# Kernel tuning notes

Hardware: AMD Instinct MI355X
Metric: run time of the kernel (lower is better)

Reference implementation:

```python
import jax, jax.numpy as jnp
import numpy as np

FULL_RANGE = 128
MOOD_DIM = 4
LAYERS = 4
UNITS = 512
MOOD_UNITS = 32


def lstm_layer(x, Wih, Whh, bih, bhh):
    # x: [B, T, I]; torch LSTM gate order: i, f, g, o
    B, T, _ = x.shape
    H = Whh.shape[1]
    xg = jnp.einsum('bti,gi->btg', x, Wih) + bih + bhh  # [B, T, 4H]

    def step(carry, g_t):
        h, c = carry
        g = g_t + h @ Whh.T
        i, f, gc, o = jnp.split(g, 4, axis=-1)
        c = jax.nn.sigmoid(f) * c + jax.nn.sigmoid(i) * jnp.tanh(gc)
        h = jax.nn.sigmoid(o) * jnp.tanh(c)
        return (h, c), h

    h0 = jnp.zeros((B, H), x.dtype)
    (_, _), hs = jax.lax.scan(step, (h0, h0), xg.transpose(1, 0, 2))
    return hs.transpose(1, 0, 2)  # [B, T, H]


def setup_inputs() -> dict:
    key = jax.random.key(0)
    ks = jax.random.split(key, 16)
    s = 0.05
    H4 = 4 * UNITS
    in0 = FULL_RANGE + MOOD_UNITS
    return {
        'inputs': jax.random.normal(ks[0], (16, 1024, FULL_RANGE), jnp.float32),
        'moods': jax.random.normal(ks[1], (16, MOOD_DIM), jnp.float32),
        'W_mood': jax.random.normal(ks[2], (MOOD_UNITS, MOOD_DIM), jnp.float32) * s,
        'b_mood': jnp.zeros((MOOD_UNITS,), jnp.float32),
        'W_ih0': jax.random.normal(ks[3], (H4, in0), jnp.float32) * s,
        'W_hh0': jax.random.normal(ks[4], (H4, UNITS), jnp.float32) * s,
        'b_ih0': jax.random.normal(ks[5], (H4,), jnp.float32) * s,
        'b_hh0': jax.random.normal(ks[6], (H4,), jnp.float32) * s,
        'W_ih_rest': jax.random.normal(ks[7], (LAYERS - 1, H4, UNITS), jnp.float32) * s,
        'W_hh_rest': jax.random.normal(ks[8], (LAYERS - 1, H4, UNITS), jnp.float32) * s,
        'b_ih_rest': jax.random.normal(ks[9], (LAYERS - 1, H4), jnp.float32) * s,
        'b_hh_rest': jax.random.normal(ks[10], (LAYERS - 1, H4), jnp.float32) * s,
        'W_out': jax.random.normal(ks[11], (FULL_RANGE, UNITS), jnp.float32) * s,
        'b_out': jnp.zeros((FULL_RANGE,), jnp.float32),
    }


def reference(inputs, moods, W_mood, b_mood, W_ih0, W_hh0, b_ih0, b_hh0,
              W_ih_rest, W_hh_rest, b_ih_rest, b_hh_rest, W_out, b_out):
    B, S, _ = inputs.shape
    m = moods @ W_mood.T + b_mood                      # [B, MOOD_UNITS]
    m = jnp.broadcast_to(m[:, None, :], (B, S, MOOD_UNITS))
    x = jnp.concatenate([inputs, m], axis=2)           # [B, S, FULL_RANGE+MOOD_UNITS]

    params = [(W_ih0, W_hh0, b_ih0, b_hh0)] + [
        (W_ih_rest[i], W_hh_rest[i], b_ih_rest[i], b_hh_rest[i])
        for i in range(LAYERS - 1)
    ]
    for i, (Wih, Whh, bih, bhh) in enumerate(params):
        prev = x
        d = 2 ** i
        F = x.shape[-1]
        # torch unfold(1,d,d).permute(0,3,1,2).view(B*d, S//d, F):
        # sub-batch (b,k) is the stride-d subsequence with phase k
        xd = x.reshape(B, S // d, d, F).transpose(0, 2, 1, 3).reshape(B * d, S // d, F)
        yd = lstm_layer(xd, Wih, Whh, bih, bhh)         # [B*d, S//d, H]
        x = yd.reshape(B, d, S // d, UNITS).transpose(0, 2, 1, 3).reshape(B, S, UNITS)
        if i > 0:
            x = prev + x
    return x @ W_out.T + b_out                          # [B, S, FULL_RANGE]
```

## Files before the change

kernel.cpp:

```cpp
#include <hip/hip_runtime.h>
#include <stdint.h>

#define DEVFN __device__ __forceinline__
#define SCOPE_AGENT __HIP_MEMORY_SCOPE_AGENT

static constexpr int B_ = 16;
static constexpr int S_ = 1024;
static constexpr int FR = 128;
static constexpr int MU = 32;
static constexpr int H_ = 512;
static constexpr int G4 = 2048;

static constexpr int NCH_WHH = 4 * 64 * 2048;
static constexpr int NCH_WI0 = 16 * 2048;
static constexpr int NCH_WIR = 3 * 64 * 2048;
static constexpr int NCH_TOT = NCH_WHH + NCH_WI0 + NCH_WIR;

static constexpr int HV64 = 128 * 256;

typedef _Float16 h2_t __attribute__((ext_vector_type(2)));

DEVFN uint16_t f2h(float x) { union { _Float16 f; uint16_t u; } c; c.f = (_Float16)x; return c.u; }
DEVFN uint32_t pack_f16(float a, float b) { return (uint32_t)f2h(a) | ((uint32_t)f2h(b) << 16); }

DEVFN float fd2(uint32_t a, uint32_t b, float c) {
#if __has_builtin(__builtin_amdgcn_fdot2)
    return __builtin_amdgcn_fdot2(__builtin_bit_cast(h2_t, a),
                                  __builtin_bit_cast(h2_t, b), c, false);
#else
    asm("v_dot2_f32_f16 %0, %1, %2, %0" : "+v"(c) : "v"(a), "v"(b));
    return c;
#endif
}
DEVFN float dot8f(uint4 w, uint4 x, float s) {
    s = fd2(w.x, x.x, s); s = fd2(w.y, x.y, s);
    s = fd2(w.z, x.z, s); s = fd2(w.w, x.w, s);
    return s;
}
DEVFN float sigm(float x) { return 1.0f / (1.0f + __expf(-x)); }
DEVFN float tanhfast(float x) {
    float e = __expf(2.0f * fabsf(x));
    float r = 1.0f - 2.0f / (e + 1.0f);
    return copysignf(r, x);
}

__global__ __launch_bounds__(256) void mood_kernel(
    const float* __restrict__ moods, const float* __restrict__ W_mood,
    const float* __restrict__ b_mood, const float* __restrict__ W_ih0,
    const float* __restrict__ b_ih0, const float* __restrict__ b_hh0,
    float* __restrict__ mc)
{
    int b = blockIdx.x, tid = threadIdx.x;
    __shared__ float m[MU];
    if (tid < MU) {
        float s = b_mood[tid];
        #pragma unroll
        for (int j = 0; j < 4; j++) s += moods[b * 4 + j] * W_mood[tid * 4 + j];
        m[tid] = s;
    }
    __syncthreads();
    for (int row = tid; row < G4; row += 256) {
        float s = b_ih0[row] + b_hh0[row];
        const float* w = W_ih0 + (size_t)row * (FR + MU) + FR;
        #pragma unroll
        for (int u = 0; u < MU; u++) s += m[u] * w[u];
        mc[(size_t)b * G4 + row] = s;
    }
}

__global__ __launch_bounds__(256) void pack_kernel(
    const float* __restrict__ W_hh0, const float* __restrict__ W_hh_r,
    const float* __restrict__ W_ih0, const float* __restrict__ W_ih_r,
    uint4* __restrict__ pwh, uint4* __restrict__ pwi0, uint4* __restrict__ pwir)
{
    int c = blockIdx.x * 256 + threadIdx.x;
    if (c >= NCH_TOT) return;
    const float* src;
    uint4* dst;
    if (c < NCH_WHH) {
        int l = c >> 17, ck = (c >> 11) & 63, row = c & 2047;
        const float* W = (l == 0) ? W_hh0 : W_hh_r + (size_t)(l - 1) * G4 * H_;
        src = W + (size_t)row * H_ + ck * 8;
        dst = pwh + c;
    } else if (c < NCH_WHH + NCH_WI0) {
        int d = c - NCH_WHH;
        int ck = d >> 11, row = d & 2047;
        src = W_ih0 + (size_t)row * (FR + MU) + ck * 8;
        dst = pwi0 + d;
    } else {
        int e = c - NCH_WHH - NCH_WI0;
        int l = e >> 17, ck = (e >> 11) & 63, row = e & 2047;
        src = W_ih_r + (size_t)l * G4 * H_ + (size_t)row * H_ + ck * 8;
        dst = pwir + e;
    }
    uint4 o;
    o.x = pack_f16(src[0], src[1]);
    o.y = pack_f16(src[2], src[3]);
    o.z = pack_f16(src[4], src[5]);
    o.w = pack_f16(src[6], src[7]);
    *dst = o;
}

#define HSTEP(J) { \
    _Pragma("unroll") \
    for (int b = 0; b < SB; b++) { \
        uint4 hv = *(const uint4*)&lds_h[b][kg * 64 + (J) * 8]; \
        accA[b] = dot8f(h0c##J, hv, accA[b]); \
        accB[b] = dot8f(h1c##J, hv, accB[b]); \
    } }

#define XBODY(J) { \
    uint4 w0 = WI0[(size_t)(J) * G4 + row0]; \
    uint4 w1 = WI0[(size_t)(J) * G4 + row1]; \
    _Pragma("unroll") \
    for (int b = 0; b < SB; b++) { \
        uint4 xv = *(const uint4*)&lds_x[b][kg * (KIN / 8) + (J) * 8]; \
        accA[b] = dot8f(w0, xv, accA[b]); \
        accB[b] = dot8f(w1, xv, accB[b]); \
    } }

template <int LAYER>
__global__ __attribute__((amdgpu_waves_per_eu(2, 2))) __launch_bounds__(512)
void scan_kernel(
    const float* x_in, float* x_out,
    const uint4* __restrict__ pwi, const uint4* __restrict__ pwh,
    const float* __restrict__ biasA, const float* __restrict__ biasB,
    unsigned long long* __restrict__ hb64, uint32_t tagbase)
{
    constexpr int DIL = 1 << LAYER;
    constexpr int SB = DIL;
    constexpr int T = S_ / DIL;
    constexpr int KIN = (LAYER == 0) ? FR : H_;
    constexpr int NJX = KIN / 64;
    constexpr int XTOT = SB * KIN;
    constexpr int XRS = (XTOT + 511) / 512;
    constexpr int KSH = (LAYER == 0) ? 7 : 9;
    constexpr int LOFF = (LAYER == 0) ? 0 : (LAYER - 1);
    constexpr bool WREG = (LAYER <= 1);
    constexpr bool EARLY = (SB <= 4);

    const int bid = blockIdx.x;
    const int g = bid & 15, wgi = bid >> 4;
    const int tid = threadIdx.x;
    const int kg = tid >> 6;
    const int r6 = tid & 63;
    const int gp = r6 >> 5;
    const int um = r6 & 31;
    const int U0 = wgi * 32;
    const int row0 = (2 * gp) * H_ + U0 + um;
    const int row1 = row0 + H_;
    const int rl0 = (2 * gp) * 32 + um, rl1 = rl0 + 32;
    const int sb0 = g * SB;

    __shared__ __align__(16) uint16_t lds_x[SB][KIN];
    __shared__ __align__(16) uint16_t lds_h[SB][H_];
    __shared__ float lds_p[SB][8][132];

    const uint4* WH = pwh + ((size_t)(LAYER * 64 + kg * 8)) * G4;

    uint4 h0c0, h1c0, h0c1, h1c1, h0c2, h1c2, h0c3, h1c3;
    uint4 h0c4, h1c4, h0c5, h1c5, h0c6, h1c6, h0c7, h1c7;
    if constexpr (WREG) {
        h0c0 = WH[(size_t)0 * G4 + row0]; h1c0 = WH[(size_t)0 * G4 + row1];
        h0c1 = WH[(size_t)1 * G4 + row0]; h1c1 = WH[(size_t)1 * G4 + row1];
        h0c2 = WH[(size_t)2 * G4 + row0]; h1c2 = WH[(size_t)2 * G4 + row1];
        h0c3 = WH[(size_t)3 * G4 + row0]; h1c3 = WH[(size_t)3 * G4 + row1];
        h0c4 = WH[(size_t)4 * G4 + row0]; h1c4 = WH[(size_t)4 * G4 + row1];
        h0c5 = WH[(size_t)5 * G4 + row0]; h1c5 = WH[(size_t)5 * G4 + row1];
        h0c6 = WH[(size_t)6 * G4 + row0]; h1c6 = WH[(size_t)6 * G4 + row1];
        h0c7 = WH[(size_t)7 * G4 + row0]; h1c7 = WH[(size_t)7 * G4 + row1];
    }

    const uint4* WI0;
    if constexpr (LAYER == 0) WI0 = pwi + ((size_t)(kg * NJX)) * G4;
    else                      WI0 = pwi + ((size_t)(LOFF * 64 + kg * 8)) * G4;

    const int b0 = tid >> 5, uu = tid & 31;
    const bool upd = tid < SB * 32;
    float biasv[4] = {0.f, 0.f, 0.f, 0.f};
    float cst = 0.0f;
    if (upd) {
        #pragma unroll
        for (int Gx = 0; Gx < 4; Gx++) {
            int RR = Gx * H_ + U0 + uu;
            if constexpr (LAYER == 0)
                biasv[Gx] = biasA[(size_t)(sb0 + b0) * G4 + RR];
            else
                biasv[Gx] = biasA[RR] + biasB[RR];
        }
    }
    const size_t pslot = (size_t)(sb0 + b0) * 256 + ((U0 + uu) >> 1);
    const int usb = sb0 + b0, ubg = usb >> LAYER, uk = usb & (DIL - 1);

    float xsr[XRS];
    #pragma unroll
    for (int rr = 0; rr < XRS; rr++) {
        int idx = tid + rr * 512;
        if (idx < XTOT) {
            int b = idx >> KSH, off = idx & (KIN - 1);
            int sb = sb0 + b, bg = sb >> LAYER, k = sb & (DIL - 1);
            xsr[rr] = x_in[((size_t)bg * S_ + k) * KIN + off];
        }
    }
    asm volatile("s_waitcnt vmcnt(0)" ::: "memory");
    __syncthreads();
    if (upd && ((uu & 1) == 0))
        __hip_atomic_store(hb64 + HV64 + pslot,
                           (unsigned long long)tagbase << 32,
                           __ATOMIC_RELAXED, SCOPE_AGENT);

    for (int t = 0; t < T; t++) {
        #pragma unroll
        for (int rr = 0; rr < XRS; rr++) {
            int idx = tid + rr * 512;
            if (idx < XTOT) lds_x[idx >> KSH][idx & (KIN - 1)] = f2h(xsr[rr]);
        }
        __syncthreads();

        const unsigned long long* hrd = hb64 + (size_t)((t + 1) & 1) * HV64;
        const uint32_t want = tagbase + (uint32_t)t;

        unsigned long long pve[EARLY ? SB : 1];
        if constexpr (EARLY) {
            if (tid < 256) {
                #pragma unroll
                for (int b = 0; b < SB; b++)
                    pve[b] = __hip_atomic_load(hrd + (size_t)(sb0 + b) * 256 + tid,
                                               __ATOMIC_RELAXED, SCOPE_AGENT);
            }
        }

        if (t + 1 < T) {
            #pragma unroll
            for (int rr = 0; rr < XRS; rr++) {
                int idx = tid + rr * 512;
                if (idx < XTOT) {
                    int b = idx >> KSH, off = idx & (KIN - 1);
                    int sb = sb0 + b, bg = sb >> LAYER, k = sb & (DIL - 1);
                    xsr[rr] = x_in[((size_t)bg * S_ + (size_t)(t + 1) * DIL + k) * KIN + off];
                }
            }
        }

        float res = 0.f;
        if constexpr (LAYER > 0) {
            if (upd)
                res = x_in[((size_t)ubg * S_ + (size_t)t * DIL + uk) * H_ + U0 + uu];
        }

        float accA[SB], accB[SB];
        #pragma unroll
        for (int b = 0; b < SB; b++) { accA[b] = 0.f; accB[b] = 0.f; }
        if constexpr (LAYER >= 2) {
            #pragma unroll 4
            for (int j = 0; j < NJX; j++) XBODY(j)
        } else {
            #pragma unroll 2
            for (int j = 0; j < NJX; j++) XBODY(j)
        }

        asm volatile("s_waitcnt vmcnt(0)" ::: "memory");

        if (tid < 256) {
            if constexpr (EARLY) {
                #pragma unroll
                for (int b = 0; b < SB; b++) {
                    unsigned long long v = pve[b];
                    while ((uint32_t)(v >> 32) != want) {
                        __builtin_amdgcn_s_sleep(1);
                        v = __hip_atomic_load(hrd + (size_t)(sb0 + b) * 256 + tid,
                                              __ATOMIC_RELAXED, SCOPE_AGENT);
                    }
                    ((uint32_t*)&lds_h[b][0])[tid] = (uint32_t)v;
                }
            } else {
                unsigned long long pv[SB];
                #pragma unroll
                for (int b = 0; b < SB; b++)
                    pv[b] = __hip_atomic_load(hrd + (size_t)(sb0 + b) * 256 + tid,
                                              __ATOMIC_RELAXED, SCOPE_AGENT);
                #pragma unroll
                for (int b = 0; b < SB; b++) {
                    while ((uint32_t)(pv[b] >> 32) != want) {
                        __builtin_amdgcn_s_sleep(1);
                        pv[b] = __hip_atomic_load(hrd + (size_t)(sb0 + b) * 256 + tid,
                                                  __ATOMIC_RELAXED, SCOPE_AGENT);
                    }
                    ((uint32_t*)&lds_h[b][0])[tid] = (uint32_t)pv[b];
                }
            }
        }
        __syncthreads();

        if constexpr (WREG) {
            HSTEP(0) HSTEP(1) HSTEP(2) HSTEP(3)
            HSTEP(4) HSTEP(5) HSTEP(6) HSTEP(7)
        } else {
            #pragma unroll 4
            for (int j = 0; j < 8; j++) {
                uint4 w0 = WH[(size_t)j * G4 + row0];
                uint4 w1 = WH[(size_t)j * G4 + row1];
                #pragma unroll
                for (int b = 0; b < SB; b++) {
                    uint4 hv = *(const uint4*)&lds_h[b][kg * 64 + j * 8];
                    accA[b] = dot8f(w0, hv, accA[b]);
                    accB[b] = dot8f(w1, hv, accB[b]);
                }
            }
        }

        #pragma unroll
        for (int b = 0; b < SB; b++) {
            lds_p[b][kg][rl0] = accA[b];
            lds_p[b][kg][rl1] = accB[b];
        }
        asm volatile("s_waitcnt vmcnt(0)" ::: "memory");
        __syncthreads();

        if (upd) {
            float gv[4];
            #pragma unroll
            for (int Gx = 0; Gx < 4; Gx++) {
                int rl = Gx * 32 + uu;
                float s = biasv[Gx];
                #pragma unroll
                for (int q = 0; q < 8; q++) s += lds_p[b0][q][rl];
                gv[Gx] = s;
            }
            float ci = sigm(gv[0]), cf = sigm(gv[1]);
            float cg = tanhfast(gv[2]), co = sigm(gv[3]);
            cst = cf * cst + ci * cg;
            float hv = co * tanhfast(cst);
            uint32_t h16 = (uint32_t)f2h(hv);
            uint32_t partner = (uint32_t)__shfl_xor((int)h16, 1);
            if ((uu & 1) == 0)
                __hip_atomic_store(hb64 + (size_t)(t & 1) * HV64 + pslot,
                                   ((unsigned long long)(tagbase + (uint32_t)t + 1) << 32) |
                                   (unsigned long long)(h16 | (partner << 16)),
                                   __ATOMIC_RELAXED, SCOPE_AGENT);
            x_out[((size_t)ubg * S_ + (size_t)t * DIL + uk) * H_ + U0 + uu] = hv + res;
        }
    }
}

__global__ __launch_bounds__(256) void out_gemm(
    const float* __restrict__ x, const float* __restrict__ Wout,
    const float* __restrict__ bout, float* __restrict__ out)
{
    __shared__ __align__(16) float xs[8][H_];
    int tid = threadIdx.x;
    size_t tok0 = (size_t)blockIdx.x * 8;
    const float4* src = (const float4*)(x + tok0 * H_);
    for (int idx = tid; idx < 8 * H_ / 4; idx += 256)
        ((float4*)xs)[idx] = src[idx];
    __syncthreads();

    int col = tid & 127, th = tid >> 7;
    int tb = th * 4;
    float a0 = 0.f, a1 = 0.f, a2 = 0.f, a3 = 0.f;
    const float4* w = (const float4*)(Wout + (size_t)col * H_);
    #pragma unroll 4
    for (int j = 0; j < H_ / 4; j++) {
        float4 wv = w[j];
        float4 x0 = ((const float4*)xs[tb + 0])[j];
        float4 x1 = ((const float4*)xs[tb + 1])[j];
        float4 x2 = ((const float4*)xs[tb + 2])[j];
        float4 x3 = ((const float4*)xs[tb + 3])[j];
        a0 = fmaf(wv.x, x0.x, a0); a0 = fmaf(wv.y, x0.y, a0); a0 = fmaf(wv.z, x0.z, a0); a0 = fmaf(wv.w, x0.w, a0);
        a1 = fmaf(wv.x, x1.x, a1); a1 = fmaf(wv.y, x1.y, a1); a1 = fmaf(wv.z, x1.z, a1); a1 = fmaf(wv.w, x1.w, a1);
        a2 = fmaf(wv.x, x2.x, a2); a2 = fmaf(wv.y, x2.y, a2); a2 = fmaf(wv.z, x2.z, a2); a2 = fmaf(wv.w, x2.w, a2);
        a3 = fmaf(wv.x, x3.x, a3); a3 = fmaf(wv.y, x3.y, a3); a3 = fmaf(wv.z, x3.z, a3); a3 = fmaf(wv.w, x3.w, a3);
    }
    float bo = bout[col];
    out[(tok0 + tb + 0) * FR + col] = a0 + bo;
    out[(tok0 + tb + 1) * FR + col] = a1 + bo;
    out[(tok0 + tb + 2) * FR + col] = a2 + bo;
    out[(tok0 + tb + 3) * FR + col] = a3 + bo;
}

extern "C" void kernel_launch(void* const* d_in, const int* in_sizes, int n_in,
                              void* d_out, int out_size, void* d_ws, size_t ws_size,
                              hipStream_t stream)
{
    const float* inputs = (const float*)d_in[0];
    const float* moods  = (const float*)d_in[1];
    const float* W_mood = (const float*)d_in[2];
    const float* b_mood = (const float*)d_in[3];
    const float* W_ih0  = (const float*)d_in[4];
    const float* W_hh0  = (const float*)d_in[5];
    const float* b_ih0  = (const float*)d_in[6];
    const float* b_hh0  = (const float*)d_in[7];
    const float* W_ih_r = (const float*)d_in[8];
    const float* W_hh_r = (const float*)d_in[9];
    const float* b_ih_r = (const float*)d_in[10];
    const float* b_hh_r = (const float*)d_in[11];
    const float* W_out  = (const float*)d_in[12];
    const float* b_out  = (const float*)d_in[13];

    float* ws = (float*)d_ws;
    float* mc = ws;
    float* xA = ws + 32768;
    unsigned long long* hb64 = (unsigned long long*)(xA + 8388608);
    uint4* pwh  = (uint4*)(hb64 + 2 * HV64);
    uint4* pwi0 = pwh + NCH_WHH;
    uint4* pwir = pwi0 + NCH_WI0;

    (void)hipMemsetAsync(hb64, 0, 2 * HV64 * sizeof(unsigned long long), stream);
    mood_kernel<<<16, 256, 0, stream>>>(moods, W_mood, b_mood, W_ih0, b_ih0, b_hh0, mc);
    pack_kernel<<<(NCH_TOT + 255) / 256, 256, 0, stream>>>(
        W_hh0, W_hh_r, W_ih0, W_ih_r, pwh, pwi0, pwir);

    scan_kernel<0><<<256, 512, 0, stream>>>(inputs, xA, pwi0, pwh, mc, nullptr, hb64, 1u);
    scan_kernel<1><<<256, 512, 0, stream>>>(xA, xA, pwir, pwh,
                                            b_ih_r, b_hh_r, hb64, 1026u);
    scan_kernel<2><<<256, 512, 0, stream>>>(xA, xA, pwir, pwh,
                                            b_ih_r + G4, b_hh_r + G4, hb64, 1539u);
    scan_kernel<3><<<256, 512, 0, stream>>>(xA, xA, pwir, pwh,
                                            b_ih_r + 2 * G4, b_hh_r + 2 * G4, hb64, 1796u);

    out_gemm<<<2048, 256, 0, stream>>>(xA, W_out, b_out, (float*)d_out);
}
```

Before: 5.292 ms.

## Fuse LSTM layer pairs into one launch with flag-based cross-layer pipelining

Merges layers 0+1 and layers 2+3 into single launches of 512 blocks. The first layer of each pair publishes per-timestep progress flags after its atomic output stores, and the second layer spin-waits on those flags before loading its inputs. This lets the dependent layer's recurrence run concurrently with the producer's instead of waiting for a full kernel boundary. The residual input is now staged through LDS, and tags and h-buffers are separated per layer. In exchange, waves-per-EU rises from 2 to 4, which may pressure the register-resident weights. Correctness also relies on all 512 blocks being co-resident so the spin-waits cannot deadlock.

```diff
diff --git a/kernel.cpp b/kernel.cpp
--- a/kernel.cpp
+++ b/kernel.cpp
@@ -17,6 +17,7 @@
 static constexpr int NCH_TOT = NCH_WHH + NCH_WI0 + NCH_WIR;
 
 static constexpr int HV64 = 128 * 256;
+static constexpr int NXF = 16 * 16 * 16;
 
 typedef _Float16 h2_t __attribute__((ext_vector_type(2)));
 
@@ -104,7 +105,7 @@
 #define HSTEP(J) { \
     _Pragma("unroll") \
     for (int b = 0; b < SB; b++) { \
-        uint4 hv = *(const uint4*)&lds_h[b][kg * 64 + (J) * 8]; \
+        uint4 hv = *(const uint4*)&lds_h[b * H_ + kg * 64 + (J) * 8]; \
         accA[b] = dot8f(h0c##J, hv, accA[b]); \
         accB[b] = dot8f(h1c##J, hv, accB[b]); \
     } }
@@ -114,18 +115,18 @@
     uint4 w1 = WI0[(size_t)(J) * G4 + row1]; \
     _Pragma("unroll") \
     for (int b = 0; b < SB; b++) { \
-        uint4 xv = *(const uint4*)&lds_x[b][kg * (KIN / 8) + (J) * 8]; \
+        uint4 xv = *(const uint4*)&lds_x[b * KIN + kg * (KIN / 8) + (J) * 8]; \
         accA[b] = dot8f(w0, xv, accA[b]); \
         accB[b] = dot8f(w1, xv, accB[b]); \
     } }
 
 template <int LAYER>
-__global__ __attribute__((amdgpu_waves_per_eu(2, 2))) __launch_bounds__(512)
-void scan_kernel(
-    const float* x_in, float* x_out,
+DEVFN void scan_body(
+    int bid, const float* x_in, float* x_out,
     const uint4* __restrict__ pwi, const uint4* __restrict__ pwh,
     const float* __restrict__ biasA, const float* __restrict__ biasB,
-    unsigned long long* __restrict__ hb64, uint32_t tagbase)
+    unsigned long long* __restrict__ hb64, uint32_t* __restrict__ xf,
+    uint16_t* lds_x, uint16_t* lds_h, float* lds_p, float* lds_res)
 {
     constexpr int DIL = 1 << LAYER;
     constexpr int SB = DIL;
@@ -138,8 +139,10 @@
     constexpr int LOFF = (LAYER == 0) ? 0 : (LAYER - 1);
     constexpr bool WREG = (LAYER <= 1);
     constexpr bool EARLY = (SB <= 4);
-
-    const int bid = blockIdx.x;
+    constexpr bool XPROD = (LAYER == 0 || LAYER == 2);
+    constexpr bool XCONS = (LAYER == 1 || LAYER == 3);
+    constexpr uint32_t TB = 1u;
+
     const int g = bid & 15, wgi = bid >> 4;
     const int tid = threadIdx.x;
     const int kg = tid >> 6;
@@ -152,10 +155,6 @@
     const int rl0 = (2 * gp) * 32 + um, rl1 = rl0 + 32;
     const int sb0 = g * SB;
 
-    __shared__ __align__(16) uint16_t lds_x[SB][KIN];
-    __shared__ __align__(16) uint16_t lds_h[SB][H_];
-    __shared__ float lds_p[SB][8][132];
-
     const uint4* WH = pwh + ((size_t)(LAYER * 64 + kg * 8)) * G4;
 
     uint4 h0c0, h1c0, h0c1, h1c1, h0c2, h1c2, h0c3, h1c3;
@@ -191,7 +190,16 @@
     }
     const size_t pslot = (size_t)(sb0 + b0) * 256 + ((U0 + uu) >> 1);
     const int usb = sb0 + b0, ubg = usb >> LAYER, uk = usb & (DIL - 1);
-
+    const int myprod = (tid & 511) >> 5;
+
+    if constexpr (XCONS) {
+        const uint32_t* fl = xf + (g * 16 + myprod) * 16;
+        uint32_t fv = __hip_atomic_load(fl, __ATOMIC_RELAXED, SCOPE_AGENT);
+        while (fv < 2u) {
+            __builtin_amdgcn_s_sleep(1);
+            fv = __hip_atomic_load(fl, __ATOMIC_RELAXED, SCOPE_AGENT);
+        }
+    }
     float xsr[XRS];
     #pragma unroll
     for (int rr = 0; rr < XRS; rr++) {
@@ -199,26 +207,40 @@
         if (idx < XTOT) {
             int b = idx >> KSH, off = idx & (KIN - 1);
             int sb = sb0 + b, bg = sb >> LAYER, k = sb & (DIL - 1);
-            xsr[rr] = x_in[((size_t)bg * S_ + k) * KIN + off];
+            const float* src = x_in + ((size_t)bg * S_ + k) * KIN + off;
+            if constexpr (XCONS)
+                xsr[rr] = __hip_atomic_load(src, __ATOMIC_RELAXED, SCOPE_AGENT);
+            else
+                xsr[rr] = *src;
         }
     }
     asm volatile("s_waitcnt vmcnt(0)" ::: "memory");
     __syncthreads();
     if (upd && ((uu & 1) == 0))
         __hip_atomic_store(hb64 + HV64 + pslot,
-                           (unsigned long long)tagbase << 32,
+                           (unsigned long long)TB << 32,
                            __ATOMIC_RELAXED, SCOPE_AGENT);
 
     for (int t = 0; t < T; t++) {
         #pragma unroll
         for (int rr = 0; rr < XRS; rr++) {
             int idx = tid + rr * 512;
-            if (idx < XTOT) lds_x[idx >> KSH][idx & (KIN - 1)] = f2h(xsr[rr]);
+            if (idx < XTOT) {
+                int b = idx >> KSH, off = idx & (KIN - 1);
+                lds_x[b * KIN + off] = f2h(xsr[rr]);
+                if constexpr (LAYER > 0)
+                    if ((off & ~31) == U0) lds_res[b * 32 + (off & 31)] = xsr[rr];
+            }
         }
         __syncthreads();
 
+        float res = 0.f;
+        if constexpr (LAYER > 0) {
+            if (upd) res = lds_res[b0 * 32 + uu];
+        }
+
         const unsigned long long* hrd = hb64 + (size_t)((t + 1) & 1) * HV64;
-        const uint32_t want = tagbase + (uint32_t)t;
+        const uint32_t want = TB + (uint32_t)t;
 
         unsigned long long pve[EARLY ? SB : 1];
         if constexpr (EARLY) {
@@ -231,21 +253,29 @@
         }
 
         if (t + 1 < T) {
+            if constexpr (XCONS) {
+                const uint32_t* fl = xf + (g * 16 + myprod) * 16;
+                const uint32_t need = 2u * (uint32_t)(t + 2);
+                uint32_t fv = __hip_atomic_load(fl, __ATOMIC_RELAXED, SCOPE_AGENT);
+                while (fv < need) {
+                    __builtin_amdgcn_s_sleep(1);
+                    fv = __hip_atomic_load(fl, __ATOMIC_RELAXED, SCOPE_AGENT);
+                }
+            }
             #pragma unroll
             for (int rr = 0; rr < XRS; rr++) {
                 int idx = tid + rr * 512;
                 if (idx < XTOT) {
                     int b = idx >> KSH, off = idx & (KIN - 1);
                     int sb = sb0 + b, bg = sb >> LAYER, k = sb & (DIL - 1);
-                    xsr[rr] = x_in[((size_t)bg * S_ + (size_t)(t + 1) * DIL + k) * KIN + off];
+                    const float* src =
+                        x_in + ((size_t)bg * S_ + (size_t)(t + 1) * DIL + k) * KIN + off;
+                    if constexpr (XCONS)
+                        xsr[rr] = __hip_atomic_load(src, __ATOMIC_RELAXED, SCOPE_AGENT);
+                    else
+                        xsr[rr] = *src;
                 }
             }
-        }
-
-        float res = 0.f;
-        if constexpr (LAYER > 0) {
-            if (upd)
-                res = x_in[((size_t)ubg * S_ + (size_t)t * DIL + uk) * H_ + U0 + uu];
         }
 
         float accA[SB], accB[SB];
@@ -271,7 +301,7 @@
                         v = __hip_atomic_load(hrd + (size_t)(sb0 + b) * 256 + tid,
                                               __ATOMIC_RELAXED, SCOPE_AGENT);
                     }
-                    ((uint32_t*)&lds_h[b][0])[tid] = (uint32_t)v;
+                    ((uint32_t*)&lds_h[b * H_])[tid] = (uint32_t)v;
                 }
             } else {
                 unsigned long long pv[SB];
@@ -286,7 +316,7 @@
                         pv[b] = __hip_atomic_load(hrd + (size_t)(sb0 + b) * 256 + tid,
                                                   __ATOMIC_RELAXED, SCOPE_AGENT);
                     }
-                    ((uint32_t*)&lds_h[b][0])[tid] = (uint32_t)pv[b];
+                    ((uint32_t*)&lds_h[b * H_])[tid] = (uint32_t)pv[b];
                 }
             }
         }
@@ -302,7 +332,7 @@
                 uint4 w1 = WH[(size_t)j * G4 + row1];
                 #pragma unroll
                 for (int b = 0; b < SB; b++) {
-                    uint4 hv = *(const uint4*)&lds_h[b][kg * 64 + j * 8];
+                    uint4 hv = *(const uint4*)&lds_h[b * H_ + kg * 64 + j * 8];
                     accA[b] = dot8f(w0, hv, accA[b]);
                     accB[b] = dot8f(w1, hv, accB[b]);
                 }
@@ -311,8 +341,8 @@
 
         #pragma unroll
         for (int b = 0; b < SB; b++) {
-            lds_p[b][kg][rl0] = accA[b];
-            lds_p[b][kg][rl1] = accB[b];
+            lds_p[(b * 8 + kg) * 132 + rl0] = accA[b];
+            lds_p[(b * 8 + kg) * 132 + rl1] = accB[b];
         }
         asm volatile("s_waitcnt vmcnt(0)" ::: "memory");
         __syncthreads();
@@ -324,7 +354,7 @@
                 int rl = Gx * 32 + uu;
                 float s = biasv[Gx];
                 #pragma unroll
-                for (int q = 0; q < 8; q++) s += lds_p[b0][q][rl];
+                for (int q = 0; q < 8; q++) s += lds_p[(b0 * 8 + q) * 132 + rl];
                 gv[Gx] = s;
             }
             float ci = sigm(gv[0]), cf = sigm(gv[1]);
@@ -335,12 +365,46 @@
             uint32_t partner = (uint32_t)__shfl_xor((int)h16, 1);
             if ((uu & 1) == 0)
                 __hip_atomic_store(hb64 + (size_t)(t & 1) * HV64 + pslot,
-                                   ((unsigned long long)(tagbase + (uint32_t)t + 1) << 32) |
+                                   ((unsigned long long)(TB + (uint32_t)t + 1) << 32) |
                                    (unsigned long long)(h16 | (partner << 16)),
                                    __ATOMIC_RELAXED, SCOPE_AGENT);
-            x_out[((size_t)ubg * S_ + (size_t)t * DIL + uk) * H_ + U0 + uu] = hv + res;
-        }
-    }
+            float* dst = x_out + ((size_t)ubg * S_ + (size_t)t * DIL + uk) * H_ + U0 + uu;
+            if constexpr (XPROD)
+                __hip_atomic_store(dst, hv + res, __ATOMIC_RELAXED, SCOPE_AGENT);
+            else
+                *dst = hv + res;
+        }
+        if constexpr (XPROD) {
+            asm volatile("s_waitcnt vmcnt(0)" ::: "memory");
+            if constexpr (SB >= 4) __syncthreads();
+            if (tid == 0)
+                __hip_atomic_store(xf + (g * 16 + wgi) * 16, (uint32_t)(t + 1),
+                                   __ATOMIC_RELAXED, SCOPE_AGENT);
+        }
+    }
+}
+
+template <int LA, int LB>
+__global__ __attribute__((amdgpu_waves_per_eu(4, 4))) __launch_bounds__(512)
+void fused_scan(const float* xinA, float* xoutA,
+                const float* xinB, float* xoutB,
+                const uint4* __restrict__ pwiA, const uint4* __restrict__ pwiB,
+                const uint4* __restrict__ pwh,
+                const float* __restrict__ bA1, const float* __restrict__ bA2,
+                const float* __restrict__ bB1, const float* __restrict__ bB2,
+                unsigned long long* __restrict__ hb64, uint32_t* __restrict__ xf)
+{
+    constexpr int SBMX = 1 << LB;
+    __shared__ __align__(16) uint16_t s_x[SBMX * 512];
+    __shared__ __align__(16) uint16_t s_h[SBMX * 512];
+    __shared__ float s_p[SBMX * 8 * 132];
+    __shared__ float s_r[SBMX * 32];
+    if (blockIdx.x < 256)
+        scan_body<LA>((int)blockIdx.x, xinA, xoutA, pwiA, pwh, bA1, bA2,
+                      hb64 + (size_t)LA * 2 * HV64, xf, s_x, s_h, s_p, s_r);
+    else
+        scan_body<LB>((int)blockIdx.x - 256, xinB, xoutB, pwiB, pwh, bB1, bB2,
+                      hb64 + (size_t)LB * 2 * HV64, xf, s_x, s_h, s_p, s_r);
 }
 
 __global__ __launch_bounds__(256) void out_gemm(
@@ -401,22 +465,24 @@
     float* mc = ws;
     float* xA = ws + 32768;
     unsigned long long* hb64 = (unsigned long long*)(xA + 8388608);
-    uint4* pwh  = (uint4*)(hb64 + 2 * HV64);
+    uint32_t* xf0 = (uint32_t*)(hb64 + 8 * HV64);
+    uint32_t* xf2 = xf0 + NXF;
+    uint4* pwh  = (uint4*)(xf2 + NXF);
     uint4* pwi0 = pwh + NCH_WHH;
     uint4* pwir = pwi0 + NCH_WI0;
 
-    (void)hipMemsetAsync(hb64, 0, 2 * HV64 * sizeof(unsigned long long), stream);
+    (void)hipMemsetAsync(hb64, 0, 8 * HV64 * sizeof(unsigned long long)
+                                  + 2 * NXF * sizeof(uint32_t), stream);
     mood_kernel<<<16, 256, 0, stream>>>(moods, W_mood, b_mood, W_ih0, b_ih0, b_hh0, mc);
     pack_kernel<<<(NCH_TOT + 255) / 256, 256, 0, stream>>>(
         W_hh0, W_hh_r, W_ih0, W_ih_r, pwh, pwi0, pwir);
 
-    scan_kernel<0><<<256, 512, 0, stream>>>(inputs, xA, pwi0, pwh, mc, nullptr, hb64, 1u);
-    scan_kernel<1><<<256, 512, 0, stream>>>(xA, xA, pwir, pwh,
-                                            b_ih_r, b_hh_r, hb64, 1026u);
-    scan_kernel<2><<<256, 512, 0, stream>>>(xA, xA, pwir, pwh,
-                                            b_ih_r + G4, b_hh_r + G4, hb64, 1539u);
-    scan_kernel<3><<<256, 512, 0, stream>>>(xA, xA, pwir, pwh,
-                                            b_ih_r + 2 * G4, b_hh_r + 2 * G4, hb64, 1796u);
+    fused_scan<0, 1><<<512, 512, 0, stream>>>(
+        inputs, xA, xA, xA, pwi0, pwir, pwh,
+        mc, nullptr, b_ih_r, b_hh_r, hb64, xf0);
+    fused_scan<2, 3><<<512, 512, 0, stream>>>(
+        xA, xA, xA, xA, pwir, pwir, pwh,
+        b_ih_r + G4, b_hh_r + G4, b_ih_r + 2 * G4, b_hh_r + 2 * G4, hb64, xf2);
 
     out_gemm<<<2048, 256, 0, stream>>>(xA, W_out, b_out, (float*)d_out);
 }
```

New measurement: 5.079 ms. 4.0% less time.
